# Kernel optimization log

Measured on AMD Instinct MI355X. Metric: run time of the kernel, lower is better.

## Reference

```python
import jax, jax.numpy as jnp
import numpy as np

N = 10000   # num nodes (== num_features, source uses identity features)
H = 4       # attention heads
F = 128     # out_features per head (concat=False -> mean over heads)
E = 320000  # directed edges
SLOPE = 0.2 # PyG GATConv default negative_slope


def setup_inputs() -> dict:
    key = jax.random.key(0)
    ks = jax.random.split(key, 20)
    inp = {}
    inp['x'] = jax.random.normal(ks[0], (N, N), jnp.float32)
    inp['edge_index'] = jax.random.randint(ks[1], (2, E), 0, N, dtype=jnp.int64)
    dims = [N, F, F, F]
    k = 2
    for i, din in enumerate(dims):
        inp[f'W{i}'] = jax.random.normal(ks[k], (din, H * F), jnp.float32) / np.sqrt(din).astype(np.float32); k += 1
        inp[f'as{i}'] = jax.random.normal(ks[k], (H, F), jnp.float32) / np.sqrt(F).astype(np.float32); k += 1
        inp[f'ad{i}'] = jax.random.normal(ks[k], (H, F), jnp.float32) / np.sqrt(F).astype(np.float32); k += 1
        inp[f'b{i}'] = jnp.zeros((F,), jnp.float32)
    return inp


def _gat_layer(x, src, dst, W, a_src, a_dst, b):
    # x: [N, Din]; W: [Din, H*F]; a_src/a_dst: [H, F]; b: [F]
    h = (x @ W).reshape(-1, H, F)                      # [N, H, F]
    al_s = jnp.sum(h * a_src, axis=-1)                 # [N, H]
    al_d = jnp.sum(h * a_dst, axis=-1)                 # [N, H]
    e = jax.nn.leaky_relu(al_s[src] + al_d[dst], SLOPE)  # [E', H]
    # segment softmax over edges grouped by target node
    m = jax.ops.segment_max(e, dst, num_segments=N)    # [N, H]
    ex = jnp.exp(e - m[dst])
    s = jax.ops.segment_sum(ex, dst, num_segments=N)   # [N, H]
    alpha = ex / s[dst]                                 # [E', H]
    msg = h[src] * alpha[:, :, None]                    # [E', H, F]
    out = jax.ops.segment_sum(msg, dst, num_segments=N) # [N, H, F]
    return out.mean(axis=1) + b                         # concat=False: head mean + bias


def reference(x, edge_index, W0, W1, W2, W3, as0, as1, as2, as3,
              ad0, ad1, ad2, ad3, b0, b1, b2, b3):
    # add self-loops once (PyG GATConv add_self_loops=True, same each layer)
    loop = jnp.arange(N, dtype=edge_index.dtype)
    src = jnp.concatenate([edge_index[0], loop])
    dst = jnp.concatenate([edge_index[1], loop])

    h = jax.nn.relu(_gat_layer(x, src, dst, W0, as0, ad0, b0))
    h = jax.nn.relu(_gat_layer(h, src, dst, W1, as1, ad1, b1))
    h = jax.nn.relu(_gat_layer(h, src, dst, W2, as2, ad2, b2))
    z = jnp.tanh(_gat_layer(h, src, dst, W3, as3, ad3, b3))   # encode
    adj_recon = jax.nn.sigmoid(z @ z.T)                       # decode, [N, N]
    return adj_recon, z
```

## Files before the change

### kernel.cpp

```cpp
#include <hip/hip_runtime.h>

#define N_ 10000
#define H_ 4
#define F_ 128
#define HF_ 512
#define E_ 320000
#define EN_ 330000

typedef unsigned short u16;
typedef __attribute__((ext_vector_type(8))) short bf16x8;
typedef __attribute__((ext_vector_type(4))) float f32x4;

__device__ __forceinline__ u16 f2b1(float f) {
  return (u16)((__float_as_uint(f) + 0x8000u) >> 16);
}
__device__ __forceinline__ unsigned int f2b2(float a, float b) {
  unsigned int ua = __float_as_uint(a) + 0x8000u;
  unsigned int ub = __float_as_uint(b) + 0x8000u;
  return (ua >> 16) | (ub & 0xffff0000u);
}
__device__ __forceinline__ float b2f(u16 u) {
  return __uint_as_float(((unsigned int)u) << 16);
}
__device__ __forceinline__ void async_cp16(const void* g, void* l) {
  __builtin_amdgcn_global_load_lds((__attribute__((address_space(1))) void*)g,
                                   (__attribute__((address_space(3))) void*)l,
                                   16, 0, 0);
}

__global__ void transpose_f2b(const float* __restrict__ in, u16* __restrict__ out,
                              int R, int C) {
  __shared__ float t[32][33];
  int bx = blockIdx.x * 32, by = blockIdx.y * 32;
  int tx = threadIdx.x, ty = threadIdx.y;
#pragma unroll
  for (int i = 0; i < 32; i += 8) {
    int r = by + ty + i, c = bx + tx;
    if (r < R && c < C) t[ty + i][tx] = in[(size_t)r * C + c];
  }
  __syncthreads();
#pragma unroll
  for (int i = 0; i < 32; i += 8) {
    int c = bx + ty + i, r = by + tx;
    if (r < R && c < C) out[(size_t)c * R + r] = f2b1(t[tx][ty + i]);
  }
}

__global__ void zero_k(int* __restrict__ p, int n) {
  int t = blockIdx.x * blockDim.x + threadIdx.x;
  if (t < n) p[t] = 0;
}
__global__ void hist_k(const int* __restrict__ ei, int* __restrict__ cnt) {
  int t = blockIdx.x * blockDim.x + threadIdx.x;
  if (t >= EN_) return;
  int d = (t < E_) ? ei[E_ + t] : (t - E_);
  atomicAdd(&cnt[d], 1);
}
__global__ void scan_k(const int* __restrict__ cnt, int* __restrict__ rp) {
  __shared__ int l[1024];
  const int CH = 10;
  int t = threadIdx.x;
  int base = t * CH;
  int loc[CH];
  int s = 0;
#pragma unroll
  for (int i = 0; i < CH; ++i) {
    int idx = base + i;
    int c = (idx < N_) ? cnt[idx] : 0;
    loc[i] = s; s += c;
  }
  l[t] = s;
  __syncthreads();
  for (int off = 1; off < 1024; off <<= 1) {
    int v = (t >= off) ? l[t - off] : 0;
    __syncthreads();
    l[t] += v;
    __syncthreads();
  }
  int cb = (t == 0) ? 0 : l[t - 1];
#pragma unroll
  for (int i = 0; i < CH; ++i) {
    int idx = base + i;
    if (idx < N_) rp[idx] = cb + loc[i];
  }
  if (t == 1023) rp[N_] = l[1023];
}
__global__ void fill_k(const int* __restrict__ ei, const int* __restrict__ rp,
                       int* __restrict__ fl, int* __restrict__ csrc) {
  int t = blockIdx.x * blockDim.x + threadIdx.x;
  if (t >= EN_) return;
  int s, d;
  if (t < E_) { s = ei[t]; d = ei[E_ + t]; } else { s = d = t - E_; }
  int pos = rp[d] + atomicAdd(&fl[d], 1);
  csrc[pos] = s;
}

#define MFMA_STEP()                                                           \
  {                                                                           \
    bf16x8 af[4], bv[4];                                                      \
    _Pragma("unroll") for (int i = 0; i < 4; ++i)                             \
        af[i] = *(const bf16x8*)&As[(wm + i * 16 + l16) * 32 + quad * 8];     \
    _Pragma("unroll") for (int j = 0; j < 4; ++j)                             \
        bv[j] = *(const bf16x8*)&Bs[(wn + j * 16 + l16) * 32 + quad * 8];     \
    _Pragma("unroll") for (int i = 0; i < 4; ++i)                             \
        _Pragma("unroll") for (int j = 0; j < 4; ++j)                         \
            acc[i][j] = __builtin_amdgcn_mfma_f32_16x16x32_bf16(              \
                af[i], bv[j], acc[i][j], 0, 0, 0);                            \
  }

template <int ASRC, int MODE, int SPLIT>
__global__ __launch_bounds__(256) void gemm_k(const void* __restrict__ Av,
                                              const u16* __restrict__ Bt,
                                              float* __restrict__ C,
                                              int M, int Nc, int K) {
  __shared__ u16 As[128 * 32];
  __shared__ u16 Bs[128 * 32];
  const int tid = threadIdx.x;
  const int lane = tid & 63, wave = tid >> 6;
  const int wm = (wave >> 1) * 64, wn = (wave & 1) * 64;
  const int l16 = lane & 15, quad = lane >> 4;
  const int r0 = tid >> 2, kk = (tid & 3) * 8;

  int xb = blockIdx.x, yb = blockIdx.y, zb = 0;
  if (SPLIT) {
    int flat = blockIdx.x + gridDim.x * (blockIdx.y + gridDim.y * blockIdx.z);
    zb = flat % (int)gridDim.z;
    int r = flat / (int)gridDim.z;
    xb = r % (int)gridDim.x;
    yb = r / (int)gridDim.x;
  }
  const int mBase = yb * 128, nBase = xb * 128;

  int k0 = 0, k1 = K;
  if (SPLIT) {
    int Kper = ((K + (int)gridDim.z - 1) / (int)gridDim.z + 31) & ~31;
    k0 = zb * Kper;
    k1 = min(K, k0 + Kper);
    if (k0 > k1) k0 = k1;
  }
  const int len = k1 - k0;

  const u16* Ab = (const u16*)Av;
  const float* Af = (const float*)Av;

  size_t ar0 = (size_t)min(mBase + r0, M - 1);
  size_t ar1 = (size_t)min(mBase + r0 + 64, M - 1);
  size_t br0 = (size_t)min(nBase + r0, Nc - 1);
  size_t br1 = (size_t)min(nBase + r0 + 64, Nc - 1);
  const u16* pb0 = Bt + br0 * (size_t)K + k0 + kk;
  const u16* pb1 = Bt + br1 * (size_t)K + k0 + kk;
  const u16* pa0 = Ab + ar0 * (size_t)K + k0 + kk;
  const u16* pa1 = Ab + ar1 * (size_t)K + k0 + kk;
  const float* pf0 = Af + ar0 * (size_t)K + k0 + kk;
  const float* pf1 = Af + ar1 * (size_t)K + k0 + kk;
  u16* lA0 = As + wave * 512;
  u16* lA1 = As + 2048 + wave * 512;
  u16* lB0 = Bs + wave * 512;
  u16* lB1 = Bs + 2048 + wave * 512;

  f32x4 acc[4][4];
  f32x4 zr = {0.f, 0.f, 0.f, 0.f};
#pragma unroll
  for (int i = 0; i < 4; ++i)
#pragma unroll
    for (int j = 0; j < 4; ++j) acc[i][j] = zr;

  const int Lmain = len & ~31;
  for (int kb = 0; kb < Lmain; kb += 32) {
    async_cp16(pb0 + kb, lB0);
    async_cp16(pb1 + kb, lB1);
    if (ASRC == 0) {
      async_cp16(pa0 + kb, lA0);
      async_cp16(pa1 + kb, lA1);
    } else {
      float4 x0 = *(const float4*)(pf0 + kb);
      float4 x1 = *(const float4*)(pf0 + kb + 4);
      float4 x2 = *(const float4*)(pf1 + kb);
      float4 x3 = *(const float4*)(pf1 + kb + 4);
      uint4 u0 = make_uint4(f2b2(x0.x, x0.y), f2b2(x0.z, x0.w),
                            f2b2(x1.x, x1.y), f2b2(x1.z, x1.w));
      uint4 u1 = make_uint4(f2b2(x2.x, x2.y), f2b2(x2.z, x2.w),
                            f2b2(x3.x, x3.y), f2b2(x3.z, x3.w));
      *(uint4*)&As[r0 * 32 + kk] = u0;
      *(uint4*)&As[(r0 + 64) * 32 + kk] = u1;
    }
    __syncthreads();
    MFMA_STEP();
    __syncthreads();
  }
  if (len & 31) {
#pragma unroll
    for (int c = 0; c < 2; ++c) {
      size_t gr = c ? ar1 : ar0;
      size_t gb = c ? br1 : br0;
      int lrow = r0 + c * 64;
#pragma unroll
      for (int j = 0; j < 8; ++j) {
        int k = k0 + Lmain + kk + j;
        u16 av = 0, bvv = 0;
        if (k < k1) {
          av = (ASRC == 1) ? f2b1(Af[gr * (size_t)K + k]) : Ab[gr * (size_t)K + k];
          bvv = Bt[gb * (size_t)K + k];
        }
        As[lrow * 32 + kk + j] = av;
        Bs[lrow * 32 + kk + j] = bvv;
      }
    }
    __syncthreads();
    MFMA_STEP();
  }

  float* Cw = SPLIT ? (C + (size_t)zb * (size_t)M * (size_t)Nc) : C;
#pragma unroll
  for (int i = 0; i < 4; ++i)
#pragma unroll
    for (int j = 0; j < 4; ++j)
#pragma unroll
      for (int r = 0; r < 4; ++r) {
        int row = mBase + wm + i * 16 + quad * 4 + r;
        int col = nBase + wn + j * 16 + l16;
        if (row < M && col < Nc) {
          float v = acc[i][j][r];
          if (!SPLIT && MODE == 1) v = 1.f / (1.f + __expf(-v));
          Cw[(size_t)row * Nc + col] = v;
        }
      }
}

__global__ __launch_bounds__(256) void prep_k(const float* __restrict__ h,
                                              const float* __restrict__ asv,
                                              const float* __restrict__ adv,
                                              u16* __restrict__ h2,
                                              float* __restrict__ als,
                                              float* __restrict__ ald,
                                              int S, size_t zstride) {
  int wave = threadIdx.x >> 6, lane = threadIdx.x & 63;
  int node = blockIdx.x * 4 + wave;
  if (node >= N_) return;
  const float* hp = h + (size_t)node * HF_;
  float4 v0 = ((const float4*)hp)[lane * 2];
  float4 v1 = ((const float4*)hp)[lane * 2 + 1];
#pragma unroll 1
  for (int z = 1; z < S; ++z) {
    const float* pp = hp + (size_t)z * zstride;
    float4 w0 = ((const float4*)pp)[lane * 2];
    float4 w1 = ((const float4*)pp)[lane * 2 + 1];
    v0.x += w0.x; v0.y += w0.y; v0.z += w0.z; v0.w += w0.w;
    v1.x += w1.x; v1.y += w1.y; v1.z += w1.z; v1.w += w1.w;
  }
  float vv[8] = {v0.x, v0.y, v0.z, v0.w, v1.x, v1.y, v1.z, v1.w};
  uint4 pk = make_uint4(f2b2(vv[0], vv[1]), f2b2(vv[2], vv[3]),
                        f2b2(vv[4], vv[5]), f2b2(vv[6], vv[7]));
  *(uint4*)&h2[(size_t)node * HF_ + lane * 8] = pk;
  float4 a0 = ((const float4*)(asv + lane * 8))[0];
  float4 a1 = ((const float4*)(asv + lane * 8))[1];
  float4 d0 = ((const float4*)(adv + lane * 8))[0];
  float4 d1 = ((const float4*)(adv + lane * 8))[1];
  float aa[8] = {a0.x, a0.y, a0.z, a0.w, a1.x, a1.y, a1.z, a1.w};
  float dd[8] = {d0.x, d0.y, d0.z, d0.w, d1.x, d1.y, d1.z, d1.w};
  float ss = 0.f, sd = 0.f;
#pragma unroll
  for (int j = 0; j < 8; ++j) {
    ss += vv[j] * aa[j];
    sd += vv[j] * dd[j];
  }
#pragma unroll
  for (int m = 1; m <= 8; m <<= 1) {
    ss += __shfl_xor(ss, m, 64);
    sd += __shfl_xor(sd, m, 64);
  }
  if ((lane & 15) == 0) {
    int hh = lane >> 4;
    als[node * 4 + hh] = ss;
    ald[node * 4 + hh] = sd;
  }
}

__global__ __launch_bounds__(256) void agg_k(const u16* __restrict__ h2,
                                             const float* __restrict__ als,
                                             const float* __restrict__ ald,
                                             const int* __restrict__ rp,
                                             const int* __restrict__ csrc,
                                             const float* __restrict__ bias,
                                             u16* __restrict__ xout,
                                             float* __restrict__ z32, int act) {
  __shared__ float red[1024];
  __shared__ float sh[512];
  int n = blockIdx.x, t = threadIdx.x;
  int start = rp[n], end = rp[n + 1];
  int hh = t >> 6;
  float4 ad4 = *(const float4*)&ald[n * 4];
  float adh[4] = {ad4.x, ad4.y, ad4.z, ad4.w};
  float lm[4] = {-1e30f, -1e30f, -1e30f, -1e30f};
  for (int j = start + t; j < end; j += 256) {
    int s = csrc[j];
    float4 a4 = *(const float4*)&als[s * 4];
    float e0 = a4.x + adh[0]; e0 = e0 > 0.f ? e0 : 0.2f * e0;
    float e1 = a4.y + adh[1]; e1 = e1 > 0.f ? e1 : 0.2f * e1;
    float e2 = a4.z + adh[2]; e2 = e2 > 0.f ? e2 : 0.2f * e2;
    float e3 = a4.w + adh[3]; e3 = e3 > 0.f ? e3 : 0.2f * e3;
    lm[0] = fmaxf(lm[0], e0); lm[1] = fmaxf(lm[1], e1);
    lm[2] = fmaxf(lm[2], e2); lm[3] = fmaxf(lm[3], e3);
  }
#pragma unroll
  for (int h = 0; h < 4; ++h) red[t * 4 + h] = lm[h];
  __syncthreads();
  for (int off = 128; off >= 1; off >>= 1) {
    if (t < off) {
#pragma unroll
      for (int h = 0; h < 4; ++h)
        red[t * 4 + h] = fmaxf(red[t * 4 + h], red[(t + off) * 4 + h]);
    }
    __syncthreads();
  }
  float mh = red[hh];
  float adhh = adh[hh];
  float acc0 = 0.f, acc1 = 0.f, ssum = 0.f;
  for (int j = start; j < end; ++j) {
    int s = csrc[j];
    float e = als[s * 4 + hh] + adhh;
    e = e > 0.f ? e : 0.2f * e;
    float w = __expf(e - mh);
    ssum += w;
    unsigned int p = *(const unsigned int*)&h2[(size_t)s * HF_ + 2 * t];
    acc0 += w * b2f((u16)(p & 0xffffu));
    acc1 += w * b2f((u16)(p >> 16));
  }
  float inv = 1.f / ssum;
  sh[2 * t] = acc0 * inv;
  sh[2 * t + 1] = acc1 * inv;
  __syncthreads();
  if (t < 64) {
    int f0 = 2 * t, f1 = 2 * t + 1;
    float w0 = 0.25f * (sh[f0] + sh[128 + f0] + sh[256 + f0] + sh[384 + f0]) + bias[f0];
    float w1 = 0.25f * (sh[f1] + sh[128 + f1] + sh[256 + f1] + sh[384 + f1]) + bias[f1];
    if (act) { w0 = tanhf(w0); w1 = tanhf(w1); }
    else     { w0 = fmaxf(w0, 0.f); w1 = fmaxf(w1, 0.f); }
    if (z32) {
      z32[(size_t)n * F_ + f0] = w0;
      z32[(size_t)n * F_ + f1] = w1;
    }
    *(unsigned int*)&xout[(size_t)n * F_ + f0] = f2b2(w0, w1);
  }
}

extern "C" void kernel_launch(void* const* d_in, const int* in_sizes, int n_in,
                              void* d_out, int out_size, void* d_ws, size_t ws_size,
                              hipStream_t stream) {
  const float* x = (const float*)d_in[0];
  const int* ei = (const int*)d_in[1];
  const float* W[4]; const float* asv[4]; const float* adv[4]; const float* bv[4];
  for (int i = 0; i < 4; ++i) {
    W[i]   = (const float*)d_in[2 + i * 4];
    asv[i] = (const float*)d_in[3 + i * 4];
    adv[i] = (const float*)d_in[4 + i * 4];
    bv[i]  = (const float*)d_in[5 + i * 4];
  }
  float* out_adj = (float*)d_out;
  float* out_z = out_adj + (size_t)N_ * N_;

  char* w = (char*)d_ws;
  size_t o = 0;
  auto carve = [&](size_t bytes) {
    char* p = w + o;
    o += (bytes + 255) & ~(size_t)255;
    return p;
  };
  float* hbuf = (float*)carve((size_t)N_ * HF_ * 4);
  u16* h2   = (u16*)carve((size_t)N_ * HF_ * 2);
  u16* wt0  = (u16*)carve((size_t)HF_ * N_ * 2);
  u16* wt1  = (u16*)carve((size_t)HF_ * F_ * 2);
  u16* wt2  = (u16*)carve((size_t)HF_ * F_ * 2);
  u16* wt3  = (u16*)carve((size_t)HF_ * F_ * 2);
  float* als = (float*)carve((size_t)N_ * 4 * 4);
  float* ald = (float*)carve((size_t)N_ * 4 * 4);
  u16* bufA = (u16*)carve((size_t)N_ * F_ * 2);
  u16* bufB = (u16*)carve((size_t)N_ * F_ * 2);
  u16* zb   = (u16*)carve((size_t)N_ * F_ * 2);
  int* cnt = (int*)carve((size_t)2 * N_ * 4);
  int* fl = cnt + N_;
  int* rowptr = (int*)carve((size_t)(N_ + 1) * 4);
  int* csrc = (int*)carve((size_t)EN_ * 4);

  const int SPLITK = 8;
  float* part = out_adj;

  dim3 tb(32, 8);
  transpose_f2b<<<dim3(16, 313), tb, 0, stream>>>(W[0], wt0, N_, HF_);
  transpose_f2b<<<dim3(16, 4), tb, 0, stream>>>(W[1], wt1, F_, HF_);
  transpose_f2b<<<dim3(16, 4), tb, 0, stream>>>(W[2], wt2, F_, HF_);
  transpose_f2b<<<dim3(16, 4), tb, 0, stream>>>(W[3], wt3, F_, HF_);

  zero_k<<<(2 * N_ + 255) / 256, 256, 0, stream>>>(cnt, 2 * N_);
  hist_k<<<(EN_ + 255) / 256, 256, 0, stream>>>(ei, cnt);
  scan_k<<<1, 1024, 0, stream>>>(cnt, rowptr);
  fill_k<<<(EN_ + 255) / 256, 256, 0, stream>>>(ei, rowptr, fl, csrc);

  const u16* wt[4] = {wt0, wt1, wt2, wt3};
  const u16* xin[4] = {nullptr, bufA, bufB, bufA};
  u16* xout[4] = {bufA, bufB, bufA, zb};

  for (int l = 0; l < 4; ++l) {
    if (l == 0) {
      gemm_k<1, 0, 1><<<dim3(4, 79, SPLITK), 256, 0, stream>>>(x, wt0, part,
                                                               N_, HF_, N_);
      prep_k<<<N_ / 4, 256, 0, stream>>>(part, asv[0], adv[0], h2, als, ald,
                                         SPLITK, (size_t)N_ * HF_);
    } else {
      gemm_k<0, 0, 0><<<dim3(4, 79), 256, 0, stream>>>(xin[l], wt[l], hbuf,
                                                       N_, HF_, F_);
      prep_k<<<N_ / 4, 256, 0, stream>>>(hbuf, asv[l], adv[l], h2, als, ald,
                                         1, 0);
    }
    agg_k<<<N_, 256, 0, stream>>>(h2, als, ald, rowptr, csrc, bv[l], xout[l],
                                  (l == 3) ? out_z : nullptr, (l == 3) ? 1 : 0);
  }

  gemm_k<0, 1, 0><<<dim3(79, 79), 256, 0, stream>>>(zb, zb, out_adj, N_, N_, F_);
}
```

Baseline: 1.382 ms.

## Double GEMM K-tile to 64 with XOR-swizzled shared memory layout

Raises the K depth per iteration of the bf16 MFMA GEMM from 32 to 64 and stores the A and B tiles in LDS with an XOR swizzle on 16-byte chunks. Each barrier pair now covers twice as much MFMA work, and the swizzle is meant to cut bank conflicts on the fragment reads. The load mapping, the fp32-to-bf16 A path and the tail handling are reworked to match, and split-K chunks are rounded to 64. LDS use doubles, which may lower occupancy, and the single-buffered sync structure is unchanged.

```diff
diff --git a/kernel.cpp b/kernel.cpp
--- a/kernel.cpp
+++ b/kernel.cpp
@@ -95,17 +95,25 @@
   csrc[pos] = s;
 }
 
-#define MFMA_STEP()                                                           \
+#define MFMA_STEP(ASP, BSP)                                                   \
   {                                                                           \
-    bf16x8 af[4], bv[4];                                                      \
-    _Pragma("unroll") for (int i = 0; i < 4; ++i)                             \
-        af[i] = *(const bf16x8*)&As[(wm + i * 16 + l16) * 32 + quad * 8];     \
-    _Pragma("unroll") for (int j = 0; j < 4; ++j)                             \
-        bv[j] = *(const bf16x8*)&Bs[(wn + j * 16 + l16) * 32 + quad * 8];     \
-    _Pragma("unroll") for (int i = 0; i < 4; ++i)                             \
-        _Pragma("unroll") for (int j = 0; j < 4; ++j)                         \
-            acc[i][j] = __builtin_amdgcn_mfma_f32_16x16x32_bf16(              \
-                af[i], bv[j], acc[i][j], 0, 0, 0);                            \
+    _Pragma("unroll") for (int ks = 0; ks < 2; ++ks) {                        \
+      bf16x8 af[4], bv[4];                                                    \
+      _Pragma("unroll") for (int i = 0; i < 4; ++i) {                         \
+        int ra = wm + i * 16 + l16;                                           \
+        af[i] = *(const bf16x8*)&(ASP)[ra * 64 +                              \
+                                       (((ks * 4 + quad) ^ (ra & 7)) * 8)];   \
+      }                                                                       \
+      _Pragma("unroll") for (int j = 0; j < 4; ++j) {                         \
+        int rb = wn + j * 16 + l16;                                           \
+        bv[j] = *(const bf16x8*)&(BSP)[rb * 64 +                              \
+                                       (((ks * 4 + quad) ^ (rb & 7)) * 8)];   \
+      }                                                                       \
+      _Pragma("unroll") for (int i = 0; i < 4; ++i)                           \
+          _Pragma("unroll") for (int j = 0; j < 4; ++j)                       \
+              acc[i][j] = __builtin_amdgcn_mfma_f32_16x16x32_bf16(            \
+                  af[i], bv[j], acc[i][j], 0, 0, 0);                          \
+    }                                                                         \
   }
 
 template <int ASRC, int MODE, int SPLIT>
@@ -113,13 +121,12 @@
                                               const u16* __restrict__ Bt,
                                               float* __restrict__ C,
                                               int M, int Nc, int K) {
-  __shared__ u16 As[128 * 32];
-  __shared__ u16 Bs[128 * 32];
+  __shared__ u16 As[128 * 64];
+  __shared__ u16 Bs[128 * 64];
   const int tid = threadIdx.x;
   const int lane = tid & 63, wave = tid >> 6;
   const int wm = (wave >> 1) * 64, wn = (wave & 1) * 64;
   const int l16 = lane & 15, quad = lane >> 4;
-  const int r0 = tid >> 2, kk = (tid & 3) * 8;
 
   int xb = blockIdx.x, yb = blockIdx.y, zb = 0;
   if (SPLIT) {
@@ -133,7 +140,7 @@
 
   int k0 = 0, k1 = K;
   if (SPLIT) {
-    int Kper = ((K + (int)gridDim.z - 1) / (int)gridDim.z + 31) & ~31;
+    int Kper = ((K + (int)gridDim.z - 1) / (int)gridDim.z + 63) & ~63;
     k0 = zb * Kper;
     k1 = min(K, k0 + Kper);
     if (k0 > k1) k0 = k1;
@@ -143,20 +150,28 @@
   const u16* Ab = (const u16*)Av;
   const float* Af = (const float*)Av;
 
-  size_t ar0 = (size_t)min(mBase + r0, M - 1);
-  size_t ar1 = (size_t)min(mBase + r0 + 64, M - 1);
-  size_t br0 = (size_t)min(nBase + r0, Nc - 1);
-  size_t br1 = (size_t)min(nBase + r0 + 64, Nc - 1);
-  const u16* pb0 = Bt + br0 * (size_t)K + k0 + kk;
-  const u16* pb1 = Bt + br1 * (size_t)K + k0 + kk;
-  const u16* pa0 = Ab + ar0 * (size_t)K + k0 + kk;
-  const u16* pa1 = Ab + ar1 * (size_t)K + k0 + kk;
-  const float* pf0 = Af + ar0 * (size_t)K + k0 + kk;
-  const float* pf1 = Af + ar1 * (size_t)K + k0 + kk;
-  u16* lA0 = As + wave * 512;
-  u16* lA1 = As + 2048 + wave * 512;
-  u16* lB0 = Bs + wave * 512;
-  u16* lB1 = Bs + 2048 + wave * 512;
+  const u16* pB[4];
+  const u16* pA[4];
+  u16* dB[4];
+  u16* dA[4];
+#pragma unroll
+  for (int c = 0; c < 4; ++c) {
+    int slot = c * 64 + lane;
+    int rl = wave * 32 + (slot >> 3);
+    int ch = slot & 7;
+    int gcol = ((ch ^ (rl & 7)) * 8);
+    size_t gb = (size_t)min(nBase + rl, Nc - 1);
+    pB[c] = Bt + gb * (size_t)K + k0 + gcol;
+    dB[c] = Bs + wave * 2048 + c * 512;
+    if (ASRC == 0) {
+      size_t ga = (size_t)min(mBase + rl, M - 1);
+      pA[c] = Ab + ga * (size_t)K + k0 + gcol;
+      dA[c] = As + wave * 2048 + c * 512;
+    }
+  }
+  const int arow = tid >> 1, ahalf = (tid & 1) * 32;
+  size_t agr = (size_t)min(mBase + arow, M - 1);
+  const float* pfA = Af + agr * (size_t)K + k0 + ahalf;
 
   f32x4 acc[4][4];
   f32x4 zr = {0.f, 0.f, 0.f, 0.f};
@@ -165,49 +180,51 @@
 #pragma unroll
     for (int j = 0; j < 4; ++j) acc[i][j] = zr;
 
-  const int Lmain = len & ~31;
-  for (int kb = 0; kb < Lmain; kb += 32) {
-    async_cp16(pb0 + kb, lB0);
-    async_cp16(pb1 + kb, lB1);
-    if (ASRC == 0) {
-      async_cp16(pa0 + kb, lA0);
-      async_cp16(pa1 + kb, lA1);
-    } else {
-      float4 x0 = *(const float4*)(pf0 + kb);
-      float4 x1 = *(const float4*)(pf0 + kb + 4);
-      float4 x2 = *(const float4*)(pf1 + kb);
-      float4 x3 = *(const float4*)(pf1 + kb + 4);
-      uint4 u0 = make_uint4(f2b2(x0.x, x0.y), f2b2(x0.z, x0.w),
-                            f2b2(x1.x, x1.y), f2b2(x1.z, x1.w));
-      uint4 u1 = make_uint4(f2b2(x2.x, x2.y), f2b2(x2.z, x2.w),
-                            f2b2(x3.x, x3.y), f2b2(x3.z, x3.w));
-      *(uint4*)&As[r0 * 32 + kk] = u0;
-      *(uint4*)&As[(r0 + 64) * 32 + kk] = u1;
-    }
-    __syncthreads();
-    MFMA_STEP();
-    __syncthreads();
-  }
-  if (len & 31) {
-#pragma unroll
-    for (int c = 0; c < 2; ++c) {
-      size_t gr = c ? ar1 : ar0;
-      size_t gb = c ? br1 : br0;
-      int lrow = r0 + c * 64;
-#pragma unroll
-      for (int j = 0; j < 8; ++j) {
-        int k = k0 + Lmain + kk + j;
-        u16 av = 0, bvv = 0;
-        if (k < k1) {
-          av = (ASRC == 1) ? f2b1(Af[gr * (size_t)K + k]) : Ab[gr * (size_t)K + k];
-          bvv = Bt[gb * (size_t)K + k];
-        }
-        As[lrow * 32 + kk + j] = av;
-        Bs[lrow * 32 + kk + j] = bvv;
+  const int Lmain = len & ~63;
+  for (int kb = 0; kb < Lmain; kb += 64) {
+#pragma unroll
+    for (int c = 0; c < 4; ++c) {
+      async_cp16(pB[c] + kb, dB[c]);
+      if (ASRC == 0) async_cp16(pA[c] + kb, dA[c]);
+    }
+    if (ASRC == 1) {
+      float4 xv[8];
+#pragma unroll
+      for (int j = 0; j < 8; ++j) xv[j] = *(const float4*)(pfA + kb + j * 4);
+#pragma unroll
+      for (int j = 0; j < 4; ++j) {
+        uint4 u = make_uint4(
+            f2b2(xv[2 * j].x, xv[2 * j].y), f2b2(xv[2 * j].z, xv[2 * j].w),
+            f2b2(xv[2 * j + 1].x, xv[2 * j + 1].y),
+            f2b2(xv[2 * j + 1].z, xv[2 * j + 1].w));
+        int ch = (tid & 1) * 4 + j;
+        *(uint4*)&As[arow * 64 + ((ch ^ (arow & 7)) * 8)] = u;
       }
     }
     __syncthreads();
-    MFMA_STEP();
+    MFMA_STEP(As, Bs);
+    __syncthreads();
+  }
+
+  if (len & 63) {
+    int trow = tid >> 1, thalf = (tid & 1) * 32;
+    size_t gra = (size_t)min(mBase + trow, M - 1);
+    size_t grb = (size_t)min(nBase + trow, Nc - 1);
+#pragma unroll
+    for (int cc = 0; cc < 32; ++cc) {
+      int col = thalf + cc;
+      int k = k0 + Lmain + col;
+      u16 av = 0, bvv = 0;
+      if (k < k1) {
+        av = (ASRC == 1) ? f2b1(Af[gra * (size_t)K + k]) : Ab[gra * (size_t)K + k];
+        bvv = Bt[grb * (size_t)K + k];
+      }
+      int off = trow * 64 + (((col >> 3) ^ (trow & 7)) * 8) + (col & 7);
+      As[off] = av;
+      Bs[off] = bvv;
+    }
+    __syncthreads();
+    MFMA_STEP(As, Bs);
   }
 
   float* Cw = SPLIT ? (C + (size_t)zb * (size_t)M * (size_t)Nc) : C;
```

Result: no change. 1.399 ms (+1.2%).

## Aggregate one destination node per wavefront with 16-byte feature loads

Applied to the files above, without the earlier changes.

The GAT aggregation kernel now gives each destination node a single 64-lane wavefront instead of a whole 256-thread block, packing four nodes per block. Each lane loads 8 bf16 features at a time with a 16-byte vector load. The max reduction and the head-mean reduction now use wave shuffles, which removes the shared-memory tree and its many __syncthreads barriers. The trade-off is more accumulator registers per lane and load imbalance between the four nodes in a block when their degrees differ.

```diff
diff --git a/kernel.cpp b/kernel.cpp
--- a/kernel.cpp
+++ b/kernel.cpp
@@ -284,15 +284,17 @@
                                              const float* __restrict__ bias,
                                              u16* __restrict__ xout,
                                              float* __restrict__ z32, int act) {
-  __shared__ float red[1024];
-  __shared__ float sh[512];
-  int n = blockIdx.x, t = threadIdx.x;
+  int wave = threadIdx.x >> 6, lane = threadIdx.x & 63;
+  int n = blockIdx.x * 4 + wave;
+  if (n >= N_) return;
   int start = rp[n], end = rp[n + 1];
-  int hh = t >> 6;
+  int hh = lane >> 4;
+
   float4 ad4 = *(const float4*)&ald[n * 4];
   float adh[4] = {ad4.x, ad4.y, ad4.z, ad4.w};
+
   float lm[4] = {-1e30f, -1e30f, -1e30f, -1e30f};
-  for (int j = start + t; j < end; j += 256) {
+  for (int j = start + lane; j < end; j += 64) {
     int s = csrc[j];
     float4 a4 = *(const float4*)&als[s * 4];
     float e0 = a4.x + adh[0]; e0 = e0 > 0.f ? e0 : 0.2f * e0;
@@ -303,44 +305,55 @@
     lm[2] = fmaxf(lm[2], e2); lm[3] = fmaxf(lm[3], e3);
   }
 #pragma unroll
-  for (int h = 0; h < 4; ++h) red[t * 4 + h] = lm[h];
-  __syncthreads();
-  for (int off = 128; off >= 1; off >>= 1) {
-    if (t < off) {
-#pragma unroll
-      for (int h = 0; h < 4; ++h)
-        red[t * 4 + h] = fmaxf(red[t * 4 + h], red[(t + off) * 4 + h]);
-    }
-    __syncthreads();
-  }
-  float mh = red[hh];
+  for (int m = 1; m <= 32; m <<= 1) {
+#pragma unroll
+    for (int h = 0; h < 4; ++h) lm[h] = fmaxf(lm[h], __shfl_xor(lm[h], m, 64));
+  }
+  float mh = lm[hh];
   float adhh = adh[hh];
-  float acc0 = 0.f, acc1 = 0.f, ssum = 0.f;
+
+  float acc[8] = {0.f, 0.f, 0.f, 0.f, 0.f, 0.f, 0.f, 0.f};
+  float ssum = 0.f;
+  const u16* hrow = h2 + (size_t)lane * 8;
   for (int j = start; j < end; ++j) {
     int s = csrc[j];
     float e = als[s * 4 + hh] + adhh;
     e = e > 0.f ? e : 0.2f * e;
     float w = __expf(e - mh);
     ssum += w;
-    unsigned int p = *(const unsigned int*)&h2[(size_t)s * HF_ + 2 * t];
-    acc0 += w * b2f((u16)(p & 0xffffu));
-    acc1 += w * b2f((u16)(p >> 16));
+    bf16x8 pv = *(const bf16x8*)(hrow + (size_t)s * HF_);
+#pragma unroll
+    for (int k = 0; k < 8; ++k) acc[k] += w * b2f((u16)pv[k]);
   }
   float inv = 1.f / ssum;
-  sh[2 * t] = acc0 * inv;
-  sh[2 * t + 1] = acc1 * inv;
-  __syncthreads();
-  if (t < 64) {
-    int f0 = 2 * t, f1 = 2 * t + 1;
-    float w0 = 0.25f * (sh[f0] + sh[128 + f0] + sh[256 + f0] + sh[384 + f0]) + bias[f0];
-    float w1 = 0.25f * (sh[f1] + sh[128 + f1] + sh[256 + f1] + sh[384 + f1]) + bias[f1];
-    if (act) { w0 = tanhf(w0); w1 = tanhf(w1); }
-    else     { w0 = fmaxf(w0, 0.f); w1 = fmaxf(w1, 0.f); }
+#pragma unroll
+  for (int k = 0; k < 8; ++k) acc[k] *= inv;
+
+#pragma unroll
+  for (int k = 0; k < 8; ++k) {
+    acc[k] += __shfl_xor(acc[k], 16, 64);
+    acc[k] += __shfl_xor(acc[k], 32, 64);
+  }
+  if (lane < 16) {
+    int f0 = lane * 8;
+    float4 b0 = *(const float4*)(bias + f0);
+    float4 b1 = *(const float4*)(bias + f0 + 4);
+    float bb[8] = {b0.x, b0.y, b0.z, b0.w, b1.x, b1.y, b1.z, b1.w};
+    float wv[8];
+#pragma unroll
+    for (int k = 0; k < 8; ++k) {
+      float v = 0.25f * acc[k] + bb[k];
+      wv[k] = act ? tanhf(v) : fmaxf(v, 0.f);
+    }
     if (z32) {
-      z32[(size_t)n * F_ + f0] = w0;
-      z32[(size_t)n * F_ + f1] = w1;
+      float4 z0 = {wv[0], wv[1], wv[2], wv[3]};
+      float4 z1 = {wv[4], wv[5], wv[6], wv[7]};
+      *(float4*)&z32[(size_t)n * F_ + f0] = z0;
+      *(float4*)&z32[(size_t)n * F_ + f0 + 4] = z1;
     }
-    *(unsigned int*)&xout[(size_t)n * F_ + f0] = f2b2(w0, w1);
+    uint4 pk = make_uint4(f2b2(wv[0], wv[1]), f2b2(wv[2], wv[3]),
+                          f2b2(wv[4], wv[5]), f2b2(wv[6], wv[7]));
+    *(uint4*)&xout[(size_t)n * F_ + f0] = pk;
   }
 }
 
@@ -412,8 +425,9 @@
       prep_k<<<N_ / 4, 256, 0, stream>>>(hbuf, asv[l], adv[l], h2, als, ald,
                                          1, 0);
     }
-    agg_k<<<N_, 256, 0, stream>>>(h2, als, ald, rowptr, csrc, bv[l], xout[l],
-                                  (l == 3) ? out_z : nullptr, (l == 3) ? 1 : 0);
+    agg_k<<<(N_ + 3) / 4, 256, 0, stream>>>(h2, als, ald, rowptr, csrc, bv[l],
+                                            xout[l], (l == 3) ? out_z : nullptr,
+                                            (l == 3) ? 1 : 0);
   }
 
   gemm_k<0, 1, 0><<<dim3(79, 79), 256, 0, stream>>>(zb, zb, out_adj, N_, N_, F_);
```

Measured after the change: 1.282 ms. 7.2% less time.
